# Kernel optimization log

Measured on AMD Instinct MI355X. Metric: run time of the kernel, lower is better.

Reference implementation:

```python
import jax, jax.numpy as jnp
import numpy as np

N_NODES = 200000
N_EDGES = 12800000
N_FEAT = 256


def setup_inputs() -> dict:
    key = jax.random.key(0)
    k1, k2, k3, k4 = jax.random.split(key, 4)
    x = jax.random.normal(k1, (N_NODES, N_FEAT), dtype=jnp.float32)
    edge_index = jax.random.randint(k2, (2, N_EDGES), 0, N_NODES, dtype=jnp.int64)
    attrs = jax.random.uniform(k3, (N_EDGES,), dtype=jnp.float32)
    W = jax.random.normal(k4, (N_FEAT, 1), dtype=jnp.float32) * (1.0 / np.sqrt(N_FEAT))
    b = jnp.zeros((1,), dtype=jnp.float32)
    return {"x": x, "edge_index": edge_index, "attrs": attrs, "W": W, "b": b}


def reference(x, edge_index, attrs, W, b):
    # GCNConv(num_features, 1) with edge_weight=attrs, default add_self_loops=True, normalize=True
    N = x.shape[0]
    row, col = edge_index[0], edge_index[1]  # source, target
    loop = jnp.arange(N, dtype=edge_index.dtype)
    row = jnp.concatenate([row, loop])
    col = jnp.concatenate([col, loop])
    w = jnp.concatenate([attrs, jnp.ones((N,), dtype=x.dtype)])
    # symmetric normalization: deg over targets with edge weights
    deg = jax.ops.segment_sum(w, col, num_segments=N)
    dis = jnp.where(deg > 0, jax.lax.rsqrt(deg), jnp.zeros_like(deg))
    norm = dis[row] * w * dis[col]  # [E+N]
    h = x @ W  # [N, 1]
    msg = norm[:, None] * h[row]  # gather + weight, [E+N, 1]
    out = jax.ops.segment_sum(msg, col, num_segments=N) + b  # scatter-add, [N, 1]
    out = out * jnp.tanh(jax.nn.softplus(out))  # Mish
    return out.reshape(1, -1)
```

## Files before the change

kernel.cpp:

```cpp
#include <hip/hip_runtime.h>
#include <hip/hip_fp16.h>
#include <math.h>
#include <stdint.h>


#define NFEAT 256
#define SPAN 4096
#define SPAN_BITS 12
#define MAXBKT 64
#define GC_STRIDE 32
#define SEG 32
#define BCAP 266240
#define TILE 6144
#define PBT 512
#define PWAVES (PBT / 64)
#define BBT 512

__global__ void k_zero_u32(unsigned* __restrict__ p, int n) {
    int i = blockIdx.x * blockDim.x + threadIdx.x;
    if (i < n) p[i] = 0u;
}

__global__ void k_matvec(const float* __restrict__ x,
                         const float* __restrict__ W,
                         float* __restrict__ h, int N) {
    int gid  = blockIdx.x * blockDim.x + threadIdx.x;
    int node = gid >> 6;
    int lane = gid & 63;
    if (node >= N) return;
    float4 xv = ((const float4*)(x + (size_t)node * NFEAT))[lane];
    float4 wv = ((const float4*)W)[lane];
    float s = xv.x * wv.x + xv.y * wv.y + xv.z * wv.z + xv.w * wv.w;
#pragma unroll
    for (int off = 32; off > 0; off >>= 1)
        s += __shfl_down(s, off, 64);
    if (lane == 0) h[node] = s;
}

__global__ void __launch_bounds__(PBT) k_partition(
        const int* __restrict__ row, const int* __restrict__ col,
        const float* __restrict__ attrs,
        unsigned* __restrict__ g_cnt,
        unsigned* __restrict__ keys, __half* __restrict__ att16,
        int E, int nbkt) {
    __shared__ unsigned whist[PWAVES][MAXBKT];
    __shared__ unsigned lhist[MAXBKT];
    __shared__ unsigned lstart[MAXBKT];
    __shared__ unsigned lbase[MAXBKT];
    __shared__ unsigned lkey[TILE];
    __shared__ unsigned short latt[TILE];

    const int tid  = threadIdx.x;
    const int wave = tid >> 6;
    const int e0   = blockIdx.x * TILE;
    const int e1   = min(e0 + TILE, E);
    const int nv   = (e1 - e0) & ~3;

    ((unsigned*)whist)[tid] = 0u;
    __syncthreads();
    unsigned* myh = whist[wave];
    for (int o = tid << 2; o < nv; o += PBT << 2) {
        int4 c4 = *(const int4*)(col + e0 + o);
        atomicAdd(&myh[((unsigned)c4.x) >> SPAN_BITS], 1u);
        atomicAdd(&myh[((unsigned)c4.y) >> SPAN_BITS], 1u);
        atomicAdd(&myh[((unsigned)c4.z) >> SPAN_BITS], 1u);
        atomicAdd(&myh[((unsigned)c4.w) >> SPAN_BITS], 1u);
    }
    for (int e = e0 + nv + tid; e < e1; e += PBT)
        atomicAdd(&myh[((unsigned)col[e]) >> SPAN_BITS], 1u);
    __syncthreads();
    if (tid < MAXBKT) {
        unsigned s = 0;
#pragma unroll
        for (int w = 0; w < PWAVES; ++w) {
            unsigned c = whist[w][tid];
            whist[w][tid] = s;
            s += c;
        }
        lhist[tid] = s;
    }
    __syncthreads();
    if (tid == 0) {
        unsigned s = 0;
        for (int b = 0; b < nbkt; ++b) { lstart[b] = s; s += lhist[b]; }
    }
    if (tid < nbkt) lbase[tid] = atomicAdd(&g_cnt[tid * GC_STRIDE], lhist[tid]);
    __syncthreads();
    if ((tid & 63) < nbkt) whist[wave][tid & 63] += lstart[tid & 63];
    __syncthreads();

    for (int o = tid << 2; o < nv; o += PBT << 2) {
        const int e = e0 + o;
        int4   c4 = *(const int4*)(col + e);
        int4   r4 = *(const int4*)(row + e);
        float4 a4 = *(const float4*)(attrs + e);
        {
            unsigned c = (unsigned)c4.x, bkt = c >> SPAN_BITS;
            unsigned t = atomicAdd(&myh[bkt], 1u);
            lkey[t] = ((unsigned)r4.x << SPAN_BITS) | (c & (SPAN - 1));
            latt[t] = __half_as_ushort(__float2half(a4.x));
        }
        {
            unsigned c = (unsigned)c4.y, bkt = c >> SPAN_BITS;
            unsigned t = atomicAdd(&myh[bkt], 1u);
            lkey[t] = ((unsigned)r4.y << SPAN_BITS) | (c & (SPAN - 1));
            latt[t] = __half_as_ushort(__float2half(a4.y));
        }
        {
            unsigned c = (unsigned)c4.z, bkt = c >> SPAN_BITS;
            unsigned t = atomicAdd(&myh[bkt], 1u);
            lkey[t] = ((unsigned)r4.z << SPAN_BITS) | (c & (SPAN - 1));
            latt[t] = __half_as_ushort(__float2half(a4.z));
        }
        {
            unsigned c = (unsigned)c4.w, bkt = c >> SPAN_BITS;
            unsigned t = atomicAdd(&myh[bkt], 1u);
            lkey[t] = ((unsigned)r4.w << SPAN_BITS) | (c & (SPAN - 1));
            latt[t] = __half_as_ushort(__float2half(a4.w));
        }
    }
    for (int e = e0 + nv + tid; e < e1; e += PBT) {
        unsigned c   = (unsigned)col[e];
        unsigned bkt = c >> SPAN_BITS;
        unsigned t   = atomicAdd(&myh[bkt], 1u);
        lkey[t] = ((unsigned)row[e] << SPAN_BITS) | (c & (SPAN - 1));
        latt[t] = __half_as_ushort(__float2half(attrs[e]));
    }
    __syncthreads();

    const int lane = tid & 63;
    for (int b = wave; b < nbkt; b += PWAVES) {
        const unsigned cnt = lhist[b];
        const unsigned gb  = lbase[b];
        const unsigned ls  = lstart[b];
        const size_t base  = (size_t)b * BCAP;
        for (unsigned i = lane; i < cnt; i += 64) {
            unsigned t = gb + i;
            if (t < BCAP) {
                keys[base + t]  = lkey[ls + i];
                att16[base + t] = __ushort_as_half(latt[ls + i]);
            }
        }
    }
}

__global__ void __launch_bounds__(BBT) k_bucket_deg(
        const unsigned* __restrict__ g_cnt, const unsigned* __restrict__ keys,
        const __half* __restrict__ att16, float* __restrict__ rep, int npad) {
    __shared__ float acc[SPAN];
    const int seg = blockIdx.x, bkt = blockIdx.y, tid = threadIdx.x;
#pragma unroll
    for (int j = tid; j < SPAN; j += BBT) acc[j] = 0.f;
    __syncthreads();
    const unsigned cnt = min(g_cnt[bkt * GC_STRIDE], (unsigned)BCAP);
    const unsigned per = (((cnt + SEG - 1) / SEG) + 7u) & ~7u;
    const unsigned i0 = seg * per, i1 = min(cnt, i0 + per);
    const size_t base = (size_t)bkt * BCAP;
    if (i1 > i0) {
        const unsigned count = i1 - i0;
        const unsigned nvec  = count & ~7u;
        const unsigned* kp = keys + base + i0;
        const unsigned short* ap = (const unsigned short*)att16 + base + i0;
        for (unsigned o = tid << 3; o < nvec; o += BBT << 3) {
            uint4 ka = *(const uint4*)(kp + o);
            uint4 kb = *(const uint4*)(kp + o + 4);
            uint4 av = *(const uint4*)(const void*)(ap + o);
            atomicAdd(&acc[ka.x & (SPAN - 1)],
                      __half2float(__ushort_as_half((unsigned short)(av.x & 0xffffu))));
            atomicAdd(&acc[ka.y & (SPAN - 1)],
                      __half2float(__ushort_as_half((unsigned short)(av.x >> 16))));
            atomicAdd(&acc[ka.z & (SPAN - 1)],
                      __half2float(__ushort_as_half((unsigned short)(av.y & 0xffffu))));
            atomicAdd(&acc[ka.w & (SPAN - 1)],
                      __half2float(__ushort_as_half((unsigned short)(av.y >> 16))));
            atomicAdd(&acc[kb.x & (SPAN - 1)],
                      __half2float(__ushort_as_half((unsigned short)(av.z & 0xffffu))));
            atomicAdd(&acc[kb.y & (SPAN - 1)],
                      __half2float(__ushort_as_half((unsigned short)(av.z >> 16))));
            atomicAdd(&acc[kb.z & (SPAN - 1)],
                      __half2float(__ushort_as_half((unsigned short)(av.w & 0xffffu))));
            atomicAdd(&acc[kb.w & (SPAN - 1)],
                      __half2float(__ushort_as_half((unsigned short)(av.w >> 16))));
        }
        for (unsigned i = nvec + tid; i < count; i += BBT)
            atomicAdd(&acc[kp[i] & (SPAN - 1)],
                      __half2float(__ushort_as_half(ap[i])));
    }
    __syncthreads();
    float* dst = rep + (size_t)seg * npad + (size_t)bkt * SPAN;
#pragma unroll
    for (int j = tid; j < SPAN; j += BBT) dst[j] = acc[j];
}

__global__ void k_norm(const float* __restrict__ rep,
                       const float* __restrict__ h,
                       float* __restrict__ dis, float* __restrict__ g,
                       int N, int npad) {
    int n = blockIdx.x * blockDim.x + threadIdx.x;
    if (n >= N) return;
    float d = 1.0f;
#pragma unroll
    for (int s = 0; s < SEG; ++s) d += rep[(size_t)s * npad + n];
    float si = rsqrtf(d);
    dis[n] = si;
    g[n]   = si * h[n];
}

__global__ void __launch_bounds__(BBT) k_bucket_scatter(
        const unsigned* __restrict__ g_cnt, const unsigned* __restrict__ keys,
        const __half* __restrict__ att16, const float* __restrict__ g,
        float* __restrict__ rep, int npad) {
    __shared__ float acc[SPAN];
    const int seg = blockIdx.x, bkt = blockIdx.y, tid = threadIdx.x;
#pragma unroll
    for (int j = tid; j < SPAN; j += BBT) acc[j] = 0.f;
    __syncthreads();
    const unsigned cnt = min(g_cnt[bkt * GC_STRIDE], (unsigned)BCAP);
    const unsigned per = (((cnt + SEG - 1) / SEG) + 7u) & ~7u;
    const unsigned i0 = seg * per, i1 = min(cnt, i0 + per);
    const size_t base = (size_t)bkt * BCAP;
    if (i1 > i0) {
        const unsigned count = i1 - i0;
        const unsigned nvec  = count & ~7u;
        const unsigned* kp = keys + base + i0;
        const unsigned short* ap = (const unsigned short*)att16 + base + i0;
        for (unsigned o = tid << 3; o < nvec; o += BBT << 3) {
            uint4 ka = *(const uint4*)(kp + o);
            uint4 kb = *(const uint4*)(kp + o + 4);
            uint4 av = *(const uint4*)(const void*)(ap + o);
            float g0 = g[ka.x >> SPAN_BITS];
            float g1 = g[ka.y >> SPAN_BITS];
            float g2 = g[ka.z >> SPAN_BITS];
            float g3 = g[ka.w >> SPAN_BITS];
            float g4 = g[kb.x >> SPAN_BITS];
            float g5 = g[kb.y >> SPAN_BITS];
            float g6 = g[kb.z >> SPAN_BITS];
            float g7 = g[kb.w >> SPAN_BITS];
            float a0 = __half2float(__ushort_as_half((unsigned short)(av.x & 0xffffu)));
            float a1 = __half2float(__ushort_as_half((unsigned short)(av.x >> 16)));
            float a2 = __half2float(__ushort_as_half((unsigned short)(av.y & 0xffffu)));
            float a3 = __half2float(__ushort_as_half((unsigned short)(av.y >> 16)));
            float a4 = __half2float(__ushort_as_half((unsigned short)(av.z & 0xffffu)));
            float a5 = __half2float(__ushort_as_half((unsigned short)(av.z >> 16)));
            float a6 = __half2float(__ushort_as_half((unsigned short)(av.w & 0xffffu)));
            float a7 = __half2float(__ushort_as_half((unsigned short)(av.w >> 16)));
            atomicAdd(&acc[ka.x & (SPAN - 1)], a0 * g0);
            atomicAdd(&acc[ka.y & (SPAN - 1)], a1 * g1);
            atomicAdd(&acc[ka.z & (SPAN - 1)], a2 * g2);
            atomicAdd(&acc[ka.w & (SPAN - 1)], a3 * g3);
            atomicAdd(&acc[kb.x & (SPAN - 1)], a4 * g4);
            atomicAdd(&acc[kb.y & (SPAN - 1)], a5 * g5);
            atomicAdd(&acc[kb.z & (SPAN - 1)], a6 * g6);
            atomicAdd(&acc[kb.w & (SPAN - 1)], a7 * g7);
        }
        for (unsigned i = nvec + tid; i < count; i += BBT) {
            unsigned k = kp[i];
            atomicAdd(&acc[k & (SPAN - 1)],
                      __half2float(__ushort_as_half(ap[i])) * g[k >> SPAN_BITS]);
        }
    }
    __syncthreads();
    float* dst = rep + (size_t)seg * npad + (size_t)bkt * SPAN;
#pragma unroll
    for (int j = tid; j < SPAN; j += BBT) dst[j] = acc[j];
}

__global__ void k_final(const float* __restrict__ rep,
                        const float* __restrict__ dis,
                        const float* __restrict__ g,
                        const float* __restrict__ b,
                        float* __restrict__ out, int N, int npad) {
    int n = blockIdx.x * blockDim.x + threadIdx.x;
    if (n >= N) return;
    float s = 0.f;
#pragma unroll
    for (int k = 0; k < SEG; ++k) s += rep[(size_t)k * npad + n];
    float v  = dis[n] * (s + g[n]) + b[0];
    float sp = (v > 20.0f) ? v : log1pf(expf(v));
    out[n] = v * tanhf(sp);
}

__global__ void f_deg(const int* __restrict__ col, const float* __restrict__ attrs,
                      float* __restrict__ deg, int E) {
    int e = blockIdx.x * blockDim.x + threadIdx.x;
    if (e < E) atomicAdd(deg + col[e], attrs[e]);
}
__global__ void f_init(float* __restrict__ deg, int N) {
    int n = blockIdx.x * blockDim.x + threadIdx.x;
    if (n < N) deg[n] = 1.0f;
}
__global__ void f_norm(float* deg_dis, float* hg, float* __restrict__ acc, int N) {
    int n = blockIdx.x * blockDim.x + threadIdx.x;
    if (n >= N) return;
    float s = rsqrtf(deg_dis[n]);
    float gv = s * hg[n];
    deg_dis[n] = s; hg[n] = gv; acc[n] = s * gv;
}
__global__ void f_scatter(const int* __restrict__ row, const int* __restrict__ col,
                          const float* __restrict__ attrs, const float* __restrict__ g,
                          const float* __restrict__ dis, float* __restrict__ acc, int E) {
    int e = blockIdx.x * blockDim.x + threadIdx.x;
    if (e < E) atomicAdd(acc + col[e], attrs[e] * g[row[e]] * dis[col[e]]);
}
__global__ void f_mish(float* out, const float* __restrict__ b, int N) {
    int n = blockIdx.x * blockDim.x + threadIdx.x;
    if (n >= N) return;
    float v = out[n] + b[0];
    float sp = (v > 20.0f) ? v : log1pf(expf(v));
    out[n] = v * tanhf(sp);
}

extern "C" void kernel_launch(void* const* d_in, const int* in_sizes, int n_in,
                              void* d_out, int out_size, void* d_ws, size_t ws_size,
                              hipStream_t stream) {
    const float* x     = (const float*)d_in[0];
    const int*   ei    = (const int*)d_in[1];
    const float* attrs = (const float*)d_in[2];
    const float* W     = (const float*)d_in[3];
    const float* bias  = (const float*)d_in[4];
    float* out = (float*)d_out;

    const int N = in_sizes[0] / NFEAT;
    const int E = in_sizes[1] / 2;
    const int* row = ei;
    const int* col = ei + E;

    const int nbkt = (N + SPAN - 1) / SPAN;
    const int npad = nbkt * SPAN;

    const size_t need = (size_t)3 * N * 4
                      + (size_t)SEG * npad * 4
                      + (size_t)MAXBKT * GC_STRIDE * 4
                      + (size_t)nbkt * BCAP * 6 + 256;
    const int BT = 256;

    if (ws_size >= need && nbkt <= MAXBKT) {
        float* h   = (float*)d_ws;
        float* dis = h + N;
        float* g   = dis + N;
        float* rep = g + N;
        unsigned* g_cnt = (unsigned*)(rep + (size_t)SEG * npad);
        unsigned* keys  = g_cnt + MAXBKT * GC_STRIDE;
        __half* att16   = (__half*)(keys + (size_t)nbkt * BCAP);

        const int pgrid = (E + TILE - 1) / TILE;

        k_zero_u32<<<(MAXBKT * GC_STRIDE + 63) / 64, 64, 0, stream>>>(
            g_cnt, MAXBKT * GC_STRIDE);
        k_matvec<<<(N + 3) / 4, BT, 0, stream>>>(x, W, h, N);
        k_partition<<<pgrid, PBT, 0, stream>>>(row, col, attrs, g_cnt,
                                               keys, att16, E, nbkt);
        dim3 bg(SEG, nbkt);
        k_bucket_deg<<<bg, BBT, 0, stream>>>(g_cnt, keys, att16, rep, npad);
        k_norm<<<(N + BT - 1) / BT, BT, 0, stream>>>(rep, h, dis, g, N, npad);
        k_bucket_scatter<<<bg, BBT, 0, stream>>>(g_cnt, keys, att16, g, rep, npad);
        k_final<<<(N + BT - 1) / BT, BT, 0, stream>>>(rep, dis, g, bias, out, N, npad);
    } else {
        float* h   = (float*)d_ws;
        float* deg = h + N;
        k_matvec<<<(N + 3) / 4, BT, 0, stream>>>(x, W, h, N);
        f_init<<<(N + BT - 1) / BT, BT, 0, stream>>>(deg, N);
        f_deg<<<(E + BT - 1) / BT, BT, 0, stream>>>(col, attrs, deg, E);
        f_norm<<<(N + BT - 1) / BT, BT, 0, stream>>>(deg, h, out, N);
        f_scatter<<<(E + BT - 1) / BT, BT, 0, stream>>>(row, col, attrs, h, deg, out, E);
        f_mish<<<(N + BT - 1) / BT, BT, 0, stream>>>(out, bias, N);
    }
}
```

Baseline: 562.2 us.

## Fuse deg/norm/scatter/final phases into one cooperative persistent kernel with grid syncs

```diff
diff --git a/kernel.cpp b/kernel.cpp
--- a/kernel.cpp
+++ b/kernel.cpp
@@ -1,7 +1,10 @@
 #include <hip/hip_runtime.h>
 #include <hip/hip_fp16.h>
+#include <hip/hip_cooperative_groups.h>
 #include <math.h>
 #include <stdint.h>
+
+namespace cg = cooperative_groups;
 
 
 #define NFEAT 256
@@ -144,11 +147,11 @@
     }
 }
 
-__global__ void __launch_bounds__(BBT) k_bucket_deg(
+__device__ __forceinline__ void deg_task(
+        int seg, int bkt, int tid,
         const unsigned* __restrict__ g_cnt, const unsigned* __restrict__ keys,
-        const __half* __restrict__ att16, float* __restrict__ rep, int npad) {
-    __shared__ float acc[SPAN];
-    const int seg = blockIdx.x, bkt = blockIdx.y, tid = threadIdx.x;
+        const unsigned short* __restrict__ att_all,
+        float* __restrict__ rep, int npad, float* acc) {
 #pragma unroll
     for (int j = tid; j < SPAN; j += BBT) acc[j] = 0.f;
     __syncthreads();
@@ -160,7 +163,7 @@
         const unsigned count = i1 - i0;
         const unsigned nvec  = count & ~7u;
         const unsigned* kp = keys + base + i0;
-        const unsigned short* ap = (const unsigned short*)att16 + base + i0;
+        const unsigned short* ap = att_all + base + i0;
         for (unsigned o = tid << 3; o < nvec; o += BBT << 3) {
             uint4 ka = *(const uint4*)(kp + o);
             uint4 kb = *(const uint4*)(kp + o + 4);
@@ -190,28 +193,14 @@
     float* dst = rep + (size_t)seg * npad + (size_t)bkt * SPAN;
 #pragma unroll
     for (int j = tid; j < SPAN; j += BBT) dst[j] = acc[j];
-}
-
-__global__ void k_norm(const float* __restrict__ rep,
-                       const float* __restrict__ h,
-                       float* __restrict__ dis, float* __restrict__ g,
-                       int N, int npad) {
-    int n = blockIdx.x * blockDim.x + threadIdx.x;
-    if (n >= N) return;
-    float d = 1.0f;
-#pragma unroll
-    for (int s = 0; s < SEG; ++s) d += rep[(size_t)s * npad + n];
-    float si = rsqrtf(d);
-    dis[n] = si;
-    g[n]   = si * h[n];
-}
-
-__global__ void __launch_bounds__(BBT) k_bucket_scatter(
+    __syncthreads();
+}
+
+__device__ __forceinline__ void scatter_task(
+        int seg, int bkt, int tid,
         const unsigned* __restrict__ g_cnt, const unsigned* __restrict__ keys,
-        const __half* __restrict__ att16, const float* __restrict__ g,
-        float* __restrict__ rep, int npad) {
-    __shared__ float acc[SPAN];
-    const int seg = blockIdx.x, bkt = blockIdx.y, tid = threadIdx.x;
+        const unsigned short* __restrict__ att_all, const float* __restrict__ g,
+        float* __restrict__ rep, int npad, float* acc) {
 #pragma unroll
     for (int j = tid; j < SPAN; j += BBT) acc[j] = 0.f;
     __syncthreads();
@@ -223,7 +212,7 @@
         const unsigned count = i1 - i0;
         const unsigned nvec  = count & ~7u;
         const unsigned* kp = keys + base + i0;
-        const unsigned short* ap = (const unsigned short*)att16 + base + i0;
+        const unsigned short* ap = att_all + base + i0;
         for (unsigned o = tid << 3; o < nvec; o += BBT << 3) {
             uint4 ka = *(const uint4*)(kp + o);
             uint4 kb = *(const uint4*)(kp + o + 4);
@@ -263,6 +252,76 @@
     float* dst = rep + (size_t)seg * npad + (size_t)bkt * SPAN;
 #pragma unroll
     for (int j = tid; j < SPAN; j += BBT) dst[j] = acc[j];
+    __syncthreads();
+}
+
+__global__ void __launch_bounds__(BBT, 4) k_mega(
+        const unsigned* __restrict__ g_cnt, const unsigned* __restrict__ keys,
+        const __half* __restrict__ att16, const float* __restrict__ h,
+        const float* __restrict__ bias,
+        float* __restrict__ rep, float* __restrict__ dis,
+        float* __restrict__ g, float* __restrict__ out,
+        int N, int npad, int nbkt) {
+    __shared__ float acc[SPAN];
+    cg::grid_group grid = cg::this_grid();
+    const int tid = threadIdx.x;
+    const int ntask = SEG * nbkt;
+    const unsigned short* att_all = (const unsigned short*)att16;
+
+    for (int t = blockIdx.x; t < ntask; t += gridDim.x)
+        deg_task(t % SEG, t / SEG, tid, g_cnt, keys, att_all, rep, npad, acc);
+    grid.sync();
+    for (int n = blockIdx.x * BBT + tid; n < N; n += gridDim.x * BBT) {
+        float d = 1.0f;
+#pragma unroll
+        for (int s = 0; s < SEG; ++s) d += rep[(size_t)s * npad + n];
+        float si = rsqrtf(d);
+        dis[n] = si;
+        g[n]   = si * h[n];
+    }
+    grid.sync();
+    for (int t = blockIdx.x; t < ntask; t += gridDim.x)
+        scatter_task(t % SEG, t / SEG, tid, g_cnt, keys, att_all, g, rep, npad, acc);
+    grid.sync();
+    for (int n = blockIdx.x * BBT + tid; n < N; n += gridDim.x * BBT) {
+        float s = 0.f;
+#pragma unroll
+        for (int k = 0; k < SEG; ++k) s += rep[(size_t)k * npad + n];
+        float v  = dis[n] * (s + g[n]) + bias[0];
+        float sp = (v > 20.0f) ? v : log1pf(expf(v));
+        out[n] = v * tanhf(sp);
+    }
+}
+
+__global__ void __launch_bounds__(BBT) k_bucket_deg(
+        const unsigned* __restrict__ g_cnt, const unsigned* __restrict__ keys,
+        const __half* __restrict__ att16, float* __restrict__ rep, int npad) {
+    __shared__ float acc[SPAN];
+    deg_task(blockIdx.x, blockIdx.y, threadIdx.x, g_cnt, keys,
+             (const unsigned short*)att16, rep, npad, acc);
+}
+
+__global__ void k_norm(const float* __restrict__ rep,
+                       const float* __restrict__ h,
+                       float* __restrict__ dis, float* __restrict__ g,
+                       int N, int npad) {
+    int n = blockIdx.x * blockDim.x + threadIdx.x;
+    if (n >= N) return;
+    float d = 1.0f;
+#pragma unroll
+    for (int s = 0; s < SEG; ++s) d += rep[(size_t)s * npad + n];
+    float si = rsqrtf(d);
+    dis[n] = si;
+    g[n]   = si * h[n];
+}
+
+__global__ void __launch_bounds__(BBT) k_bucket_scatter(
+        const unsigned* __restrict__ g_cnt, const unsigned* __restrict__ keys,
+        const __half* __restrict__ att16, const float* __restrict__ g,
+        float* __restrict__ rep, int npad) {
+    __shared__ float acc[SPAN];
+    scatter_task(blockIdx.x, blockIdx.y, threadIdx.x, g_cnt, keys,
+                 (const unsigned short*)att16, g, rep, npad, acc);
 }
 
 __global__ void k_final(const float* __restrict__ rep,
@@ -350,11 +409,48 @@
         k_matvec<<<(N + 3) / 4, BT, 0, stream>>>(x, W, h, N);
         k_partition<<<pgrid, PBT, 0, stream>>>(row, col, attrs, g_cnt,
                                                keys, att16, E, nbkt);
-        dim3 bg(SEG, nbkt);
-        k_bucket_deg<<<bg, BBT, 0, stream>>>(g_cnt, keys, att16, rep, npad);
-        k_norm<<<(N + BT - 1) / BT, BT, 0, stream>>>(rep, h, dis, g, N, npad);
-        k_bucket_scatter<<<bg, BBT, 0, stream>>>(g_cnt, keys, att16, g, rep, npad);
-        k_final<<<(N + BT - 1) / BT, BT, 0, stream>>>(rep, dis, g, bias, out, N, npad);
+
+        static int s_cus = 0, s_coop = -1;
+        if (s_coop < 0) {
+            hipDeviceProp_t prop;
+            int dev = 0;
+            hipGetDevice(&dev);
+            if (hipGetDeviceProperties(&prop, dev) == hipSuccess) {
+                s_cus  = prop.multiProcessorCount;
+                s_coop = prop.cooperativeLaunch ? 1 : 0;
+            } else { s_cus = 256; s_coop = 0; }
+        }
+        bool launched = false;
+        if (s_coop == 1) {
+            int occ = 0;
+            if (hipOccupancyMaxActiveBlocksPerMultiprocessor(
+                    &occ, k_mega, BBT, 0) == hipSuccess && occ > 0) {
+                int blocks = occ * s_cus;
+                const int ntask = SEG * nbkt;
+                if (blocks > ntask) blocks = ntask;
+                const unsigned* p_gc = g_cnt; const unsigned* p_k = keys;
+                const __half* p_a = att16; const float* p_h = h;
+                const float* p_b = bias;
+                float* p_rep = rep; float* p_dis = dis; float* p_g = g;
+                float* p_out = out;
+                int vN = N, vnpad = npad, vnbkt = nbkt;
+                void* kargs[] = {&p_gc, &p_k, &p_a, &p_h, &p_b, &p_rep,
+                                 &p_dis, &p_g, &p_out, &vN, &vnpad, &vnbkt};
+                if (hipLaunchCooperativeKernel((const void*)k_mega,
+                        dim3(blocks), dim3(BBT), kargs, 0, stream)
+                    == hipSuccess)
+                    launched = true;
+            }
+        }
+        if (!launched) {
+            dim3 bg(SEG, nbkt);
+            k_bucket_deg<<<bg, BBT, 0, stream>>>(g_cnt, keys, att16, rep, npad);
+            k_norm<<<(N + BT - 1) / BT, BT, 0, stream>>>(rep, h, dis, g, N, npad);
+            k_bucket_scatter<<<bg, BBT, 0, stream>>>(g_cnt, keys, att16, g,
+                                                     rep, npad);
+            k_final<<<(N + BT - 1) / BT, BT, 0, stream>>>(rep, dis, g, bias,
+                                                          out, N, npad);
+        }
     } else {
         float* h   = (float*)d_ws;
         float* deg = h + N;
```

After: 747.1 us. +32.9%, slower.
